# Optimization experiments

Measured on AMD Instinct MI355X. Metric: run time of the kernel, lower is better.

The kernel has to match this reference:

```python
import jax, jax.numpy as jnp
import numpy as np

B, NA, D, H = 64, 32, 128, 6  # scenes, agents/scene, out_dim, heads
N = B * NA
E = B * NA * NA


def layer_norm(x, g, b, eps=1e-5):
    m = jnp.mean(x, axis=-1, keepdims=True)
    v = jnp.var(x, axis=-1, keepdims=True)
    return (x - m) * jax.lax.rsqrt(v + eps) * g + b


def setup_inputs() -> dict:
    key = jax.random.key(0)
    ks = jax.random.split(key, 10)
    # fully-connected edges within each scene
    ids = jnp.arange(N, dtype=jnp.int32).reshape(B, NA)
    hi = jnp.broadcast_to(ids[:, :, None], (B, NA, NA)).reshape(-1)  # repeat 'd -> (d n)'
    wi = jnp.broadcast_to(ids[:, None, :], (B, NA, NA)).reshape(-1)  # repeat 'd -> (n d)'
    s_in = 1.0 / np.sqrt(D)
    s_hd = 1.0 / np.sqrt(H * D)
    return {
        'agents': jax.random.normal(ks[0], (N, D), jnp.float32),
        'hi': hi, 'wi': wi,
        'Wq': jax.random.normal(ks[1], (H * D, D), jnp.float32) * s_in,
        'gq': jnp.ones((H * D,), jnp.float32), 'bq': jnp.zeros((H * D,), jnp.float32),
        'Wk': jax.random.normal(ks[2], (H * D, D), jnp.float32) * s_in,
        'gk': jnp.ones((H * D,), jnp.float32), 'bk': jnp.zeros((H * D,), jnp.float32),
        'Wv': jax.random.normal(ks[3], (H * D, D), jnp.float32) * s_in,
        'gv': jnp.ones((H * D,), jnp.float32), 'bv': jnp.zeros((H * D,), jnp.float32),
        'Wo1': jax.random.normal(ks[4], (D, H * D), jnp.float32) * s_hd,
        'go': jnp.ones((D,), jnp.float32), 'bo': jnp.zeros((D,), jnp.float32),
        'Wo2': jax.random.normal(ks[5], (D, D), jnp.float32) * s_in,
        'W1': jax.random.normal(ks[6], (D, D), jnp.float32) * s_in,
        'gn': jnp.ones((D,), jnp.float32), 'bn': jnp.zeros((D,), jnp.float32),
        'W2': jax.random.normal(ks[7], (D, D), jnp.float32) * s_in,
    }


def reference(agents, hi, wi, Wq, gq, bq, Wk, gk, bk, Wv, gv, bv, Wo1, go, bo, Wo2, W1, gn, bn, W2):
    n, d = agents.shape
    scale = d ** -0.5
    xh = agents[hi]                                   # [E, D]
    xw = agents[wi]                                   # [E, D]
    q = layer_norm(xh @ Wq.T, gq, bq).reshape(-1, H, d)                 # [E, H, D]
    k = layer_norm(xw @ Wk.T, gk, bk).reshape(-1, H, d)
    v = jax.nn.relu(layer_norm(xw @ Wv.T, gv, bv)).reshape(-1, H, d)
    att = jnp.sum(q * k, axis=-1) * scale             # [E, H] per-edge score
    att = jnp.exp(att - jnp.max(att))                 # global max, as in original
    att_sum = jax.ops.segment_sum(att, hi, num_segments=n)   # [N, H]
    att = att / att_sum[hi]
    out = jax.ops.segment_sum(att[..., None] * v, hi, num_segments=n)   # [N, H, D]
    out = out.reshape(n, H * d)
    out = jax.nn.relu(layer_norm(out @ Wo1.T, go, bo)) @ Wo2.T          # to_out
    nodes = agents @ W1.T
    nodes = jax.nn.relu(layer_norm(nodes + out, gn, bn))
    nodes = nodes @ W2.T
    return jax.nn.relu(nodes + agents)
```

## Files before the change

kernel.cpp:

```cpp
#include <hip/hip_runtime.h>
#include <math.h>

#define NN 2048
#define HH 6
#define HD 768
#define NA 32
#define NB 64

typedef __bf16 bf16x8 __attribute__((ext_vector_type(8)));
typedef float  f32x4  __attribute__((ext_vector_type(4)));

__device__ __forceinline__ void split2(float f, ushort& h, ushort& l) {
    const uint u = __float_as_uint(f);
    h = (ushort)(u >> 16);
    const float hf = __uint_as_float((uint)h << 16);
    l = (ushort)(__float_as_uint(f - hf) >> 16);
}

__device__ __forceinline__ bf16x8 pack8(const ushort* s) {
    uint4 u;
    u.x = (uint)s[0] | ((uint)s[1] << 16);
    u.y = (uint)s[2] | ((uint)s[3] << 16);
    u.z = (uint)s[4] | ((uint)s[5] << 16);
    u.w = (uint)s[6] | ((uint)s[7] << 16);
    return *(bf16x8*)&u;
}

__device__ __forceinline__ void ln8_split(
    const float* __restrict__ x, float mu, float rs,
    const float* __restrict__ g, const float* __restrict__ b,
    bf16x8& hi, bf16x8& lo)
{
    const float4 x0 = *(const float4*)x;
    const float4 x1 = *(const float4*)(x + 4);
    const float4 g0 = *(const float4*)g;
    const float4 g1 = *(const float4*)(g + 4);
    const float4 b0 = *(const float4*)b;
    const float4 b1 = *(const float4*)(b + 4);
    ushort hh[8], ll[8];
    float v;
    v = (x0.x - mu) * rs * g0.x + b0.x; split2(v, hh[0], ll[0]);
    v = (x0.y - mu) * rs * g0.y + b0.y; split2(v, hh[1], ll[1]);
    v = (x0.z - mu) * rs * g0.z + b0.z; split2(v, hh[2], ll[2]);
    v = (x0.w - mu) * rs * g0.w + b0.w; split2(v, hh[3], ll[3]);
    v = (x1.x - mu) * rs * g1.x + b1.x; split2(v, hh[4], ll[4]);
    v = (x1.y - mu) * rs * g1.y + b1.y; split2(v, hh[5], ll[5]);
    v = (x1.z - mu) * rs * g1.z + b1.z; split2(v, hh[6], ll[6]);
    v = (x1.w - mu) * rs * g1.w + b1.w; split2(v, hh[7], ll[7]);
    hi = pack8(hh); lo = pack8(ll);
}

__global__ __launch_bounds__(256) void split_kernel(
    const float* __restrict__ agents, const float* __restrict__ Wq,
    const float* __restrict__ Wk, const float* __restrict__ Wv,
    const float* __restrict__ Wo1, const float* __restrict__ Wo2,
    const float* __restrict__ W1, const float* __restrict__ W2,
    ushort* __restrict__ Ahi, ushort* __restrict__ Alo,
    ushort* __restrict__ Whi, ushort* __restrict__ Wlo,
    ushort* __restrict__ Wo1hi, ushort* __restrict__ Wo1lo,
    ushort* __restrict__ Wo2hi, ushort* __restrict__ Wo2lo,
    ushort* __restrict__ W1hi, ushort* __restrict__ W1lo,
    ushort* __restrict__ W2hi, ushort* __restrict__ W2lo)
{
    const int y = blockIdx.y;
    const float* src;
    ushort *dh, *dl;
    int n4;
    switch (y) {
        case 0:  src = agents; dh = Ahi;   dl = Alo;   n4 = NN * 128 / 4;  break;
        case 1:  src = Wq;  dh = Whi;                dl = Wlo;                n4 = 768*128/4; break;
        case 2:  src = Wk;  dh = Whi + 768*128;      dl = Wlo + 768*128;      n4 = 768*128/4; break;
        case 3:  src = Wv;  dh = Whi + 2*768*128;    dl = Wlo + 2*768*128;    n4 = 768*128/4; break;
        case 4:  src = Wo1; dh = Wo1hi; dl = Wo1lo;  n4 = 128 * HD / 4;  break;
        case 5:  src = Wo2; dh = Wo2hi; dl = Wo2lo;  n4 = 128 * 128 / 4; break;
        case 6:  src = W1;  dh = W1hi;  dl = W1lo;   n4 = 128 * 128 / 4; break;
        default: src = W2;  dh = W2hi;  dl = W2lo;   n4 = 128 * 128 / 4; break;
    }
    const int i = blockIdx.x * 256 + threadIdx.x;
    if (i < n4) {
        const float4 v = ((const float4*)src)[i];
        ushort4 h, l;
        split2(v.x, h.x, l.x);
        split2(v.y, h.y, l.y);
        split2(v.z, h.z, l.z);
        split2(v.w, h.w, l.w);
        ((ushort4*)dh)[i] = h;
        ((ushort4*)dl)[i] = l;
    }
}

__global__ __launch_bounds__(256) void proj_mfma_kernel(
    const ushort* __restrict__ Ahi, const ushort* __restrict__ Alo,
    const ushort* __restrict__ Whi, const ushort* __restrict__ Wlo,
    float* __restrict__ R, float* __restrict__ ps)
{
    const int tid = threadIdx.x;
    const int wave = tid >> 6, lane = tid & 63;
    const int row0 = blockIdx.x * 64 + wave * 16;
    const int cb0  = blockIdx.y * 64;
    const int m0   = blockIdx.y / 12, pb = blockIdx.y % 12;
    const int lrow = lane & 15, kq = lane >> 4;
    const int koff = kq * 8;

    const ushort* ah = Ahi + (size_t)(row0 + lrow) * 128 + koff;
    const ushort* al = Alo + (size_t)(row0 + lrow) * 128 + koff;

    f32x4 acc[4];
    #pragma unroll
    for (int ct = 0; ct < 4; ++ct)
        #pragma unroll
        for (int j = 0; j < 4; ++j) acc[ct][j] = 0.f;

    #pragma unroll
    for (int kt = 0; kt < 4; ++kt) {
        const bf16x8 avh = *(const bf16x8*)(ah + kt * 32);
        const bf16x8 avl = *(const bf16x8*)(al + kt * 32);
        #pragma unroll
        for (int ct = 0; ct < 4; ++ct) {
            const size_t wof = (size_t)(cb0 + ct * 16 + lrow) * 128 + koff + kt * 32;
            const bf16x8 bvh = *(const bf16x8*)(Whi + wof);
            const bf16x8 bvl = *(const bf16x8*)(Wlo + wof);
            acc[ct] = __builtin_amdgcn_mfma_f32_16x16x32_bf16(avh, bvh, acc[ct], 0, 0, 0);
            acc[ct] = __builtin_amdgcn_mfma_f32_16x16x32_bf16(avh, bvl, acc[ct], 0, 0, 0);
            acc[ct] = __builtin_amdgcn_mfma_f32_16x16x32_bf16(avl, bvh, acc[ct], 0, 0, 0);
        }
    }

    const int cloc = cb0 - m0 * 768;
    #pragma unroll
    for (int ct = 0; ct < 4; ++ct) {
        const int c = cloc + ct * 16 + lrow;
        float* rp = R + ((size_t)m0 * NN + row0 + kq * 4) * HD + c;
        #pragma unroll
        for (int j = 0; j < 4; ++j)
            rp[(size_t)j * HD] = acc[ct][j];
    }

    #pragma unroll
    for (int j = 0; j < 4; ++j) {
        float sj = acc[0][j] + acc[1][j] + acc[2][j] + acc[3][j];
        float qj = acc[0][j] * acc[0][j] + acc[1][j] * acc[1][j]
                 + acc[2][j] * acc[2][j] + acc[3][j] * acc[3][j];
        #pragma unroll
        for (int msk = 1; msk <= 8; msk <<= 1) {
            sj += __shfl_xor(sj, msk);
            qj += __shfl_xor(qj, msk);
        }
        if (lrow == 0) {
            const size_t o = ((size_t)m0 * NN + row0 + kq * 4 + j) * 24 + pb * 2;
            ps[o]     = sj;
            ps[o + 1] = qj;
        }
    }
}

__global__ __launch_bounds__(64) void attn_mfma_kernel(
    const float* __restrict__ R, const float* __restrict__ ps,
    const float* __restrict__ gq, const float* __restrict__ bq,
    const float* __restrict__ gk, const float* __restrict__ bk,
    const float* __restrict__ gv, const float* __restrict__ bv,
    ushort* __restrict__ Ohi, ushort* __restrict__ Olo)
{
    __shared__ ushort phi[16][40];
    __shared__ ushort plo[16][40];
    __shared__ float stat_s[3][32][2];
    const int lane = threadIdx.x;
    const int lrow = lane & 15, kq = lane >> 4;
    const int scene = blockIdx.x, h = blockIdx.y, rt = blockIdx.z;
    const int brow = scene * 32;

    const float* Rq = R;
    const float* Rk = R + (size_t)NN * HD;
    const float* Rv = R + (size_t)2 * NN * HD;

    for (int i = lane; i < 96; i += 64) {
        const int m = i >> 5, row = i & 31;
        const float4* pv = (const float4*)(ps + ((size_t)m * NN + brow + row) * 24);
        float s = 0.f, q = 0.f;
        #pragma unroll
        for (int c = 0; c < 6; ++c) {
            const float4 v = pv[c];
            s += v.x + v.z;
            q += v.y + v.w;
        }
        const float mu  = s * (1.f / 768.f);
        const float var = q * (1.f / 768.f) - mu * mu;
        stat_s[m][row][0] = mu;
        stat_s[m][row][1] = rsqrtf(var + 1e-5f);
    }
    __syncthreads();

    const int qrow = brow + rt * 16 + lrow;
    const float muq = stat_s[0][rt * 16 + lrow][0];
    const float rsq = stat_s[0][rt * 16 + lrow][1];
    float muk[2], rsk[2];
    #pragma unroll
    for (int ct = 0; ct < 2; ++ct) {
        muk[ct] = stat_s[1][ct * 16 + lrow][0];
        rsk[ct] = stat_s[1][ct * 16 + lrow][1];
    }
    float muv[8], rsv[8];
    #pragma unroll
    for (int j = 0; j < 8; ++j) {
        muv[j] = stat_s[2][kq * 8 + j][0];
        rsv[j] = stat_s[2][kq * 8 + j][1];
    }

    f32x4 s[2];
    #pragma unroll
    for (int ct = 0; ct < 2; ++ct)
        #pragma unroll
        for (int j = 0; j < 4; ++j) s[ct][j] = 0.f;

    #pragma unroll
    for (int kt = 0; kt < 4; ++kt) {
        const int c0 = h * 128 + kt * 32 + kq * 8;
        bf16x8 qh, ql;
        ln8_split(Rq + (size_t)qrow * HD + c0, muq, rsq, gq + c0, bq + c0, qh, ql);
        #pragma unroll
        for (int ct = 0; ct < 2; ++ct) {
            bf16x8 kh, kl;
            ln8_split(Rk + (size_t)(brow + ct * 16 + lrow) * HD + c0, muk[ct], rsk[ct],
                      gk + c0, bk + c0, kh, kl);
            s[ct] = __builtin_amdgcn_mfma_f32_16x16x32_bf16(qh, kh, s[ct], 0, 0, 0);
            s[ct] = __builtin_amdgcn_mfma_f32_16x16x32_bf16(qh, kl, s[ct], 0, 0, 0);
            s[ct] = __builtin_amdgcn_mfma_f32_16x16x32_bf16(ql, kh, s[ct], 0, 0, 0);
        }
    }

    const float scl = 0.08838834764831845f;
    float p0[4], p1[4];
    #pragma unroll
    for (int j = 0; j < 4; ++j) {
        const float a = s[0][j] * scl, b = s[1][j] * scl;
        float m = fmaxf(a, b);
        #pragma unroll
        for (int msk = 1; msk <= 8; msk <<= 1) m = fmaxf(m, __shfl_xor(m, msk));
        const float ea = __expf(a - m), eb = __expf(b - m);
        float su = ea + eb;
        #pragma unroll
        for (int msk = 1; msk <= 8; msk <<= 1) su += __shfl_xor(su, msk);
        const float inv = 1.f / su;
        p0[j] = ea * inv;
        p1[j] = eb * inv;
    }

    #pragma unroll
    for (int j = 0; j < 4; ++j) {
        ushort hh, ll;
        split2(p0[j], hh, ll);
        phi[kq * 4 + j][lrow] = hh;
        plo[kq * 4 + j][lrow] = ll;
        split2(p1[j], hh, ll);
        phi[kq * 4 + j][16 + lrow] = hh;
        plo[kq * 4 + j][16 + lrow] = ll;
    }
    __syncthreads();
    const bf16x8 pah = *(const bf16x8*)&phi[lrow][kq * 8];
    const bf16x8 pal = *(const bf16x8*)&plo[lrow][kq * 8];

    #pragma unroll
    for (int dt = 0; dt < 8; ++dt) {
        const int d = h * 128 + dt * 16 + lrow;
        const float gvd = gv[d], bvd = bv[d];
        ushort vh[8], vl[8];
        #pragma unroll
        for (int j = 0; j < 8; ++j) {
            const float x = Rv[(size_t)(brow + kq * 8 + j) * HD + d];
            const float v = fmaxf((x - muv[j]) * rsv[j] * gvd + bvd, 0.f);
            split2(v, vh[j], vl[j]);
        }
        const bf16x8 bh = pack8(vh), bl = pack8(vl);
        f32x4 o;
        #pragma unroll
        for (int j = 0; j < 4; ++j) o[j] = 0.f;
        o = __builtin_amdgcn_mfma_f32_16x16x32_bf16(pah, bh, o, 0, 0, 0);
        o = __builtin_amdgcn_mfma_f32_16x16x32_bf16(pah, bl, o, 0, 0, 0);
        o = __builtin_amdgcn_mfma_f32_16x16x32_bf16(pal, bh, o, 0, 0, 0);
        #pragma unroll
        for (int j = 0; j < 4; ++j) {
            const size_t oo = (size_t)(brow + rt * 16 + kq * 4 + j) * HD + d;
            ushort hh, ll;
            split2(o[j], hh, ll);
            Ohi[oo] = hh;
            Olo[oo] = ll;
        }
    }
}

__global__ __launch_bounds__(256) void wo1_mfma_kernel(
    const ushort* __restrict__ Ohi, const ushort* __restrict__ Olo,
    const ushort* __restrict__ Wo1hi, const ushort* __restrict__ Wo1lo,
    float* __restrict__ P)
{
    const int tid = threadIdx.x;
    const int wave = tid >> 6, lane = tid & 63;
    const int row0 = blockIdx.x * 64 + wave * 16;
    const int col0 = blockIdx.y * 16;
    const int kb   = blockIdx.z * 256;
    const int lrow = lane & 15, kq = lane >> 4;
    const int koff = kq * 8;

    const ushort* ah = Ohi   + (size_t)(row0 + lrow) * HD + kb + koff;
    const ushort* al = Olo   + (size_t)(row0 + lrow) * HD + kb + koff;
    const ushort* bh = Wo1hi + (size_t)(col0 + lrow) * HD + kb + koff;
    const ushort* bl = Wo1lo + (size_t)(col0 + lrow) * HD + kb + koff;

    f32x4 acc;
    #pragma unroll
    for (int j = 0; j < 4; ++j) acc[j] = 0.f;

    #pragma unroll
    for (int kt = 0; kt < 8; ++kt) {
        const bf16x8 avh = *(const bf16x8*)(ah + kt * 32);
        const bf16x8 avl = *(const bf16x8*)(al + kt * 32);
        const bf16x8 bvh = *(const bf16x8*)(bh + kt * 32);
        const bf16x8 bvl = *(const bf16x8*)(bl + kt * 32);
        acc = __builtin_amdgcn_mfma_f32_16x16x32_bf16(avh, bvh, acc, 0, 0, 0);
        acc = __builtin_amdgcn_mfma_f32_16x16x32_bf16(avh, bvl, acc, 0, 0, 0);
        acc = __builtin_amdgcn_mfma_f32_16x16x32_bf16(avl, bvh, acc, 0, 0, 0);
    }

    float* pp = P + ((size_t)blockIdx.z * NN + row0 + kq * 4) * 128 + col0 + lrow;
    #pragma unroll
    for (int j = 0; j < 4; ++j)
        pp[(size_t)j * 128] = acc[j];
}

__global__ __launch_bounds__(256) void epilogue_mfma_kernel(
    const float* __restrict__ P,
    const ushort* __restrict__ Ahi, const ushort* __restrict__ Alo,
    const float* __restrict__ agents,
    const float* __restrict__ go, const float* __restrict__ bo,
    const ushort* __restrict__ Wo2hi, const ushort* __restrict__ Wo2lo,
    const ushort* __restrict__ W1hi, const ushort* __restrict__ W1lo,
    const float* __restrict__ gn, const float* __restrict__ bn,
    const ushort* __restrict__ W2hi, const ushort* __restrict__ W2lo,
    float* __restrict__ out)
{
    __shared__ float zb[16][132];
    __shared__ float red2[4][16][2];
    const int tid = threadIdx.x;
    const int wave = tid >> 6, lane = tid & 63;
    const int lrow = lane & 15, kq = lane >> 4;
    const int n0 = blockIdx.x * 16;
    const int nodeA = n0 + lrow;

    float tv[4][8];
    float s = 0.f, q = 0.f;
    #pragma unroll
    for (int kt = 0; kt < 4; ++kt) {
        const int c0 = kt * 32 + kq * 8;
        const float* pp0 = P + (size_t)nodeA * 128 + c0;
        const float* pp1 = pp0 + (size_t)NN * 128;
        const float* pp2 = pp1 + (size_t)NN * 128;
        #pragma unroll
        for (int hf = 0; hf < 2; ++hf) {
            const float4 a = *(const float4*)(pp0 + hf * 4);
            const float4 b = *(const float4*)(pp1 + hf * 4);
            const float4 c = *(const float4*)(pp2 + hf * 4);
            tv[kt][hf * 4 + 0] = a.x + b.x + c.x;
            tv[kt][hf * 4 + 1] = a.y + b.y + c.y;
            tv[kt][hf * 4 + 2] = a.z + b.z + c.z;
            tv[kt][hf * 4 + 3] = a.w + b.w + c.w;
        }
        #pragma unroll
        for (int j = 0; j < 8; ++j) { s += tv[kt][j]; q += tv[kt][j] * tv[kt][j]; }
    }
    s += __shfl_xor(s, 16); s += __shfl_xor(s, 32);
    q += __shfl_xor(q, 16); q += __shfl_xor(q, 32);
    const float mu = s * (1.f / 128.f);
    const float rs = rsqrtf(q * (1.f / 128.f) - mu * mu + 1e-5f);

    bf16x8 th[4], tl[4], ah[4], al[4];
    #pragma unroll
    for (int kt = 0; kt < 4; ++kt) {
        const int c0 = kt * 32 + kq * 8;
        const float4 g0 = *(const float4*)(go + c0);
        const float4 g1 = *(const float4*)(go + c0 + 4);
        const float4 b0 = *(const float4*)(bo + c0);
        const float4 b1 = *(const float4*)(bo + c0 + 4);
        const float gg[8] = {g0.x, g0.y, g0.z, g0.w, g1.x, g1.y, g1.z, g1.w};
        const float bb[8] = {b0.x, b0.y, b0.z, b0.w, b1.x, b1.y, b1.z, b1.w};
        ushort hh[8], ll[8];
        #pragma unroll
        for (int j = 0; j < 8; ++j) {
            const float v = fmaxf((tv[kt][j] - mu) * rs * gg[j] + bb[j], 0.f);
            split2(v, hh[j], ll[j]);
        }
        th[kt] = pack8(hh); tl[kt] = pack8(ll);
        ah[kt] = *(const bf16x8*)(Ahi + (size_t)nodeA * 128 + c0);
        al[kt] = *(const bf16x8*)(Alo + (size_t)nodeA * 128 + c0);
    }

    f32x4 u[2];
    #pragma unroll
    for (int ct2 = 0; ct2 < 2; ++ct2)
        #pragma unroll
        for (int j = 0; j < 4; ++j) u[ct2][j] = 0.f;

    #pragma unroll
    for (int ct2 = 0; ct2 < 2; ++ct2) {
        const int ct = wave * 2 + ct2;
        const size_t wb = (size_t)(ct * 16 + lrow) * 128;
        #pragma unroll
        for (int kt = 0; kt < 4; ++kt) {
            const int c0 = kt * 32 + kq * 8;
            const bf16x8 wh = *(const bf16x8*)(Wo2hi + wb + c0);
            const bf16x8 wl = *(const bf16x8*)(Wo2lo + wb + c0);
            const bf16x8 vh = *(const bf16x8*)(W1hi + wb + c0);
            const bf16x8 vl = *(const bf16x8*)(W1lo + wb + c0);
            u[ct2] = __builtin_amdgcn_mfma_f32_16x16x32_bf16(th[kt], wh, u[ct2], 0, 0, 0);
            u[ct2] = __builtin_amdgcn_mfma_f32_16x16x32_bf16(th[kt], wl, u[ct2], 0, 0, 0);
            u[ct2] = __builtin_amdgcn_mfma_f32_16x16x32_bf16(tl[kt], wh, u[ct2], 0, 0, 0);
            u[ct2] = __builtin_amdgcn_mfma_f32_16x16x32_bf16(ah[kt], vh, u[ct2], 0, 0, 0);
            u[ct2] = __builtin_amdgcn_mfma_f32_16x16x32_bf16(ah[kt], vl, u[ct2], 0, 0, 0);
            u[ct2] = __builtin_amdgcn_mfma_f32_16x16x32_bf16(al[kt], vh, u[ct2], 0, 0, 0);
        }
    }

    #pragma unroll
    for (int j = 0; j < 4; ++j) {
        float s2 = u[0][j] + u[1][j];
        float q2 = u[0][j] * u[0][j] + u[1][j] * u[1][j];
        #pragma unroll
        for (int msk = 1; msk <= 8; msk <<= 1) {
            s2 += __shfl_xor(s2, msk);
            q2 += __shfl_xor(q2, msk);
        }
        if (lrow == 0) {
            red2[wave][kq * 4 + j][0] = s2;
            red2[wave][kq * 4 + j][1] = q2;
        }
    }
    __syncthreads();
    #pragma unroll
    for (int j = 0; j < 4; ++j) {
        const int row = kq * 4 + j;
        const float s2t = red2[0][row][0] + red2[1][row][0] + red2[2][row][0] + red2[3][row][0];
        const float q2t = red2[0][row][1] + red2[1][row][1] + red2[2][row][1] + red2[3][row][1];
        const float mu2 = s2t * (1.f / 128.f);
        const float rs2 = rsqrtf(q2t * (1.f / 128.f) - mu2 * mu2 + 1e-5f);
        #pragma unroll
        for (int ct2 = 0; ct2 < 2; ++ct2) {
            const int c = (wave * 2 + ct2) * 16 + lrow;
            zb[row][c] = fmaxf((u[ct2][j] - mu2) * rs2 * gn[c] + bn[c], 0.f);
        }
    }
    __syncthreads();

    bf16x8 zh[4], zl[4];
    #pragma unroll
    for (int kt = 0; kt < 4; ++kt) {
        const int c0 = kt * 32 + kq * 8;
        const float4 z0 = *(const float4*)&zb[lrow][c0];
        const float4 z1 = *(const float4*)&zb[lrow][c0 + 4];
        const float zz[8] = {z0.x, z0.y, z0.z, z0.w, z1.x, z1.y, z1.z, z1.w};
        ushort hh[8], ll[8];
        #pragma unroll
        for (int j = 0; j < 8; ++j) split2(zz[j], hh[j], ll[j]);
        zh[kt] = pack8(hh); zl[kt] = pack8(ll);
    }
    #pragma unroll
    for (int ct2 = 0; ct2 < 2; ++ct2) {
        const int ct = wave * 2 + ct2;
        f32x4 o;
        #pragma unroll
        for (int j = 0; j < 4; ++j) o[j] = 0.f;
        const size_t wb = (size_t)(ct * 16 + lrow) * 128;
        #pragma unroll
        for (int kt = 0; kt < 4; ++kt) {
            const int c0 = kt * 32 + kq * 8;
            const bf16x8 wh = *(const bf16x8*)(W2hi + wb + c0);
            const bf16x8 wl = *(const bf16x8*)(W2lo + wb + c0);
            o = __builtin_amdgcn_mfma_f32_16x16x32_bf16(zh[kt], wh, o, 0, 0, 0);
            o = __builtin_amdgcn_mfma_f32_16x16x32_bf16(zh[kt], wl, o, 0, 0, 0);
            o = __builtin_amdgcn_mfma_f32_16x16x32_bf16(zl[kt], wh, o, 0, 0, 0);
        }
        #pragma unroll
        for (int j = 0; j < 4; ++j) {
            const size_t oo = (size_t)(n0 + kq * 4 + j) * 128 + ct * 16 + lrow;
            out[oo] = fmaxf(o[j] + agents[oo], 0.f);
        }
    }
}

extern "C" void kernel_launch(void* const* d_in, const int* in_sizes, int n_in,
                              void* d_out, int out_size, void* d_ws, size_t ws_size,
                              hipStream_t stream) {
    (void)in_sizes; (void)n_in; (void)out_size; (void)ws_size;
    const float* agents = (const float*)d_in[0];
    const float* Wq  = (const float*)d_in[3];
    const float* gq  = (const float*)d_in[4];
    const float* bq  = (const float*)d_in[5];
    const float* Wk  = (const float*)d_in[6];
    const float* gk  = (const float*)d_in[7];
    const float* bk  = (const float*)d_in[8];
    const float* Wv  = (const float*)d_in[9];
    const float* gv  = (const float*)d_in[10];
    const float* bv  = (const float*)d_in[11];
    const float* Wo1 = (const float*)d_in[12];
    const float* go  = (const float*)d_in[13];
    const float* bo  = (const float*)d_in[14];
    const float* Wo2 = (const float*)d_in[15];
    const float* W1  = (const float*)d_in[16];
    const float* gn  = (const float*)d_in[17];
    const float* bn  = (const float*)d_in[18];
    const float* W2  = (const float*)d_in[19];
    float* out = (float*)d_out;

    float* ws = (float*)d_ws;
    float* R  = ws;
    float* Pp = R;
    float* ps = R + (size_t)3 * NN * HD;
    ushort* u = (ushort*)(ps + (size_t)3 * NN * 24);
    ushort* Ohi   = u;  u += (size_t)NN * HD;
    ushort* Olo   = u;  u += (size_t)NN * HD;
    ushort* Ahi   = u;  u += (size_t)NN * 128;
    ushort* Alo   = u;  u += (size_t)NN * 128;
    ushort* Whi   = u;  u += (size_t)3 * 768 * 128;
    ushort* Wlo   = u;  u += (size_t)3 * 768 * 128;
    ushort* Wo1hi = u;  u += (size_t)128 * HD;
    ushort* Wo1lo = u;  u += (size_t)128 * HD;
    ushort* Wo2hi = u;  u += (size_t)128 * 128;
    ushort* Wo2lo = u;  u += (size_t)128 * 128;
    ushort* W1hi  = u;  u += (size_t)128 * 128;
    ushort* W1lo  = u;  u += (size_t)128 * 128;
    ushort* W2hi  = u;  u += (size_t)128 * 128;
    ushort* W2lo  = u;  u += (size_t)128 * 128;

    split_kernel<<<dim3(256, 8), 256, 0, stream>>>(
        agents, Wq, Wk, Wv, Wo1, Wo2, W1, W2,
        Ahi, Alo, Whi, Wlo, Wo1hi, Wo1lo, Wo2hi, Wo2lo, W1hi, W1lo, W2hi, W2lo);
    proj_mfma_kernel<<<dim3(32, 36), 256, 0, stream>>>(Ahi, Alo, Whi, Wlo, R, ps);
    attn_mfma_kernel<<<dim3(64, 6, 2), 64, 0, stream>>>(R, ps, gq, bq, gk, bk, gv, bv, Ohi, Olo);
    wo1_mfma_kernel<<<dim3(32, 8, 3), 256, 0, stream>>>(Ohi, Olo, Wo1hi, Wo1lo, Pp);
    epilogue_mfma_kernel<<<128, 256, 0, stream>>>(Pp, Ahi, Alo, agents, go, bo,
                                                  Wo2hi, Wo2lo, W1hi, W1lo, gn, bn,
                                                  W2hi, W2lo, out);
}
```

Measured before the change: 160.4 us.

## Fuse attention output with per-head Wo1 projection, emitting per-head partials

Merges the attention kernel and the Wo1 GEMM into one kernel. Each block, one scene and one head with two waves of 16 query rows, keeps the attention output in shared memory, splits it to hi/lo bf16 and multiplies by that head's 128-column slice of Wo1. The Ohi/Olo round trip through global memory and a kernel launch are removed. In exchange the epilogue now sums six per-head partial buffers instead of three, and Wo1 is reread by every scene block.

```diff
diff --git a/kernel.cpp b/kernel.cpp
--- a/kernel.cpp
+++ b/kernel.cpp
@@ -154,27 +154,30 @@
     }
 }
 
-__global__ __launch_bounds__(64) void attn_mfma_kernel(
+__global__ __launch_bounds__(128) void attn_wo1_kernel(
     const float* __restrict__ R, const float* __restrict__ ps,
     const float* __restrict__ gq, const float* __restrict__ bq,
     const float* __restrict__ gk, const float* __restrict__ bk,
     const float* __restrict__ gv, const float* __restrict__ bv,
-    ushort* __restrict__ Ohi, ushort* __restrict__ Olo)
+    const ushort* __restrict__ Wo1hi, const ushort* __restrict__ Wo1lo,
+    float* __restrict__ P)
 {
-    __shared__ ushort phi[16][40];
-    __shared__ ushort plo[16][40];
     __shared__ float stat_s[3][32][2];
-    const int lane = threadIdx.x;
+    __shared__ ushort phi[2][16][40];
+    __shared__ ushort plo[2][16][40];
+    __shared__ float ob[2][16][140];
+    const int tid = threadIdx.x;
+    const int rt = tid >> 6, lane = tid & 63;
     const int lrow = lane & 15, kq = lane >> 4;
-    const int scene = blockIdx.x, h = blockIdx.y, rt = blockIdx.z;
+    const int scene = blockIdx.x, h = blockIdx.y;
     const int brow = scene * 32;
 
     const float* Rq = R;
     const float* Rk = R + (size_t)NN * HD;
     const float* Rv = R + (size_t)2 * NN * HD;
 
-    for (int i = lane; i < 96; i += 64) {
-        const int m = i >> 5, row = i & 31;
+    if (tid < 96) {
+        const int m = tid >> 5, row = tid & 31;
         const float4* pv = (const float4*)(ps + ((size_t)m * NN + brow + row) * 24);
         float s = 0.f, q = 0.f;
         #pragma unroll
@@ -249,16 +252,17 @@
     for (int j = 0; j < 4; ++j) {
         ushort hh, ll;
         split2(p0[j], hh, ll);
-        phi[kq * 4 + j][lrow] = hh;
-        plo[kq * 4 + j][lrow] = ll;
+        phi[rt][kq * 4 + j][lrow] = hh;
+        plo[rt][kq * 4 + j][lrow] = ll;
         split2(p1[j], hh, ll);
-        phi[kq * 4 + j][16 + lrow] = hh;
-        plo[kq * 4 + j][16 + lrow] = ll;
+        phi[rt][kq * 4 + j][16 + lrow] = hh;
+        plo[rt][kq * 4 + j][16 + lrow] = ll;
     }
     __syncthreads();
-    const bf16x8 pah = *(const bf16x8*)&phi[lrow][kq * 8];
-    const bf16x8 pal = *(const bf16x8*)&plo[lrow][kq * 8];
-
+    const bf16x8 pah = *(const bf16x8*)&phi[rt][lrow][kq * 8];
+    const bf16x8 pal = *(const bf16x8*)&plo[rt][lrow][kq * 8];
+
+    f32x4 o[8];
     #pragma unroll
     for (int dt = 0; dt < 8; ++dt) {
         const int d = h * 128 + dt * 16 + lrow;
@@ -271,60 +275,52 @@
             split2(v, vh[j], vl[j]);
         }
         const bf16x8 bh = pack8(vh), bl = pack8(vl);
-        f32x4 o;
-        #pragma unroll
-        for (int j = 0; j < 4; ++j) o[j] = 0.f;
-        o = __builtin_amdgcn_mfma_f32_16x16x32_bf16(pah, bh, o, 0, 0, 0);
-        o = __builtin_amdgcn_mfma_f32_16x16x32_bf16(pah, bl, o, 0, 0, 0);
-        o = __builtin_amdgcn_mfma_f32_16x16x32_bf16(pal, bh, o, 0, 0, 0);
-        #pragma unroll
-        for (int j = 0; j < 4; ++j) {
-            const size_t oo = (size_t)(brow + rt * 16 + kq * 4 + j) * HD + d;
-            ushort hh, ll;
-            split2(o[j], hh, ll);
-            Ohi[oo] = hh;
-            Olo[oo] = ll;
-        }
-    }
-}
-
-__global__ __launch_bounds__(256) void wo1_mfma_kernel(
-    const ushort* __restrict__ Ohi, const ushort* __restrict__ Olo,
-    const ushort* __restrict__ Wo1hi, const ushort* __restrict__ Wo1lo,
-    float* __restrict__ P)
-{
-    const int tid = threadIdx.x;
-    const int wave = tid >> 6, lane = tid & 63;
-    const int row0 = blockIdx.x * 64 + wave * 16;
-    const int col0 = blockIdx.y * 16;
-    const int kb   = blockIdx.z * 256;
-    const int lrow = lane & 15, kq = lane >> 4;
-    const int koff = kq * 8;
-
-    const ushort* ah = Ohi   + (size_t)(row0 + lrow) * HD + kb + koff;
-    const ushort* al = Olo   + (size_t)(row0 + lrow) * HD + kb + koff;
-    const ushort* bh = Wo1hi + (size_t)(col0 + lrow) * HD + kb + koff;
-    const ushort* bl = Wo1lo + (size_t)(col0 + lrow) * HD + kb + koff;
-
-    f32x4 acc;
-    #pragma unroll
-    for (int j = 0; j < 4; ++j) acc[j] = 0.f;
-
-    #pragma unroll
-    for (int kt = 0; kt < 8; ++kt) {
-        const bf16x8 avh = *(const bf16x8*)(ah + kt * 32);
-        const bf16x8 avl = *(const bf16x8*)(al + kt * 32);
-        const bf16x8 bvh = *(const bf16x8*)(bh + kt * 32);
-        const bf16x8 bvl = *(const bf16x8*)(bl + kt * 32);
-        acc = __builtin_amdgcn_mfma_f32_16x16x32_bf16(avh, bvh, acc, 0, 0, 0);
-        acc = __builtin_amdgcn_mfma_f32_16x16x32_bf16(avh, bvl, acc, 0, 0, 0);
-        acc = __builtin_amdgcn_mfma_f32_16x16x32_bf16(avl, bvh, acc, 0, 0, 0);
-    }
-
-    float* pp = P + ((size_t)blockIdx.z * NN + row0 + kq * 4) * 128 + col0 + lrow;
-    #pragma unroll
-    for (int j = 0; j < 4; ++j)
-        pp[(size_t)j * 128] = acc[j];
+        #pragma unroll
+        for (int j = 0; j < 4; ++j) o[dt][j] = 0.f;
+        o[dt] = __builtin_amdgcn_mfma_f32_16x16x32_bf16(pah, bh, o[dt], 0, 0, 0);
+        o[dt] = __builtin_amdgcn_mfma_f32_16x16x32_bf16(pah, bl, o[dt], 0, 0, 0);
+        o[dt] = __builtin_amdgcn_mfma_f32_16x16x32_bf16(pal, bh, o[dt], 0, 0, 0);
+    }
+
+    #pragma unroll
+    for (int dt = 0; dt < 8; ++dt)
+        #pragma unroll
+        for (int j = 0; j < 4; ++j)
+            ob[rt][kq * 4 + j][dt * 16 + lrow] = o[dt][j];
+    __syncthreads();
+
+    bf16x8 oh[4], ol[4];
+    #pragma unroll
+    for (int kt = 0; kt < 4; ++kt) {
+        const float4 z0 = *(const float4*)&ob[rt][lrow][kt * 32 + kq * 8];
+        const float4 z1 = *(const float4*)&ob[rt][lrow][kt * 32 + kq * 8 + 4];
+        const float zz[8] = {z0.x, z0.y, z0.z, z0.w, z1.x, z1.y, z1.z, z1.w};
+        ushort hh[8], ll[8];
+        #pragma unroll
+        for (int j = 0; j < 8; ++j) split2(zz[j], hh[j], ll[j]);
+        oh[kt] = pack8(hh); ol[kt] = pack8(ll);
+    }
+
+    #pragma unroll
+    for (int ct = 0; ct < 8; ++ct) {
+        f32x4 p2;
+        #pragma unroll
+        for (int j = 0; j < 4; ++j) p2[j] = 0.f;
+        const size_t wb = (size_t)(ct * 16 + lrow) * HD + h * 128;
+        #pragma unroll
+        for (int kt = 0; kt < 4; ++kt) {
+            const int c0 = kt * 32 + kq * 8;
+            const bf16x8 wh = *(const bf16x8*)(Wo1hi + wb + c0);
+            const bf16x8 wl = *(const bf16x8*)(Wo1lo + wb + c0);
+            p2 = __builtin_amdgcn_mfma_f32_16x16x32_bf16(oh[kt], wh, p2, 0, 0, 0);
+            p2 = __builtin_amdgcn_mfma_f32_16x16x32_bf16(oh[kt], wl, p2, 0, 0, 0);
+            p2 = __builtin_amdgcn_mfma_f32_16x16x32_bf16(ol[kt], wh, p2, 0, 0, 0);
+        }
+        float* pp = P + ((size_t)h * NN + brow + rt * 16 + kq * 4) * 128 + ct * 16 + lrow;
+        #pragma unroll
+        for (int j = 0; j < 4; ++j)
+            pp[(size_t)j * 128] = p2[j];
+    }
 }
 
 __global__ __launch_bounds__(256) void epilogue_mfma_kernel(
@@ -351,18 +347,19 @@
     #pragma unroll
     for (int kt = 0; kt < 4; ++kt) {
         const int c0 = kt * 32 + kq * 8;
-        const float* pp0 = P + (size_t)nodeA * 128 + c0;
-        const float* pp1 = pp0 + (size_t)NN * 128;
-        const float* pp2 = pp1 + (size_t)NN * 128;
+        const size_t base = (size_t)nodeA * 128 + c0;
         #pragma unroll
         for (int hf = 0; hf < 2; ++hf) {
-            const float4 a = *(const float4*)(pp0 + hf * 4);
-            const float4 b = *(const float4*)(pp1 + hf * 4);
-            const float4 c = *(const float4*)(pp2 + hf * 4);
-            tv[kt][hf * 4 + 0] = a.x + b.x + c.x;
-            tv[kt][hf * 4 + 1] = a.y + b.y + c.y;
-            tv[kt][hf * 4 + 2] = a.z + b.z + c.z;
-            tv[kt][hf * 4 + 3] = a.w + b.w + c.w;
+            float ax = 0.f, ay = 0.f, az = 0.f, aw = 0.f;
+            #pragma unroll
+            for (int head = 0; head < 6; ++head) {
+                const float4 v = *(const float4*)(P + (size_t)head * NN * 128 + base + hf * 4);
+                ax += v.x; ay += v.y; az += v.z; aw += v.w;
+            }
+            tv[kt][hf * 4 + 0] = ax;
+            tv[kt][hf * 4 + 1] = ay;
+            tv[kt][hf * 4 + 2] = az;
+            tv[kt][hf * 4 + 3] = aw;
         }
         #pragma unroll
         for (int j = 0; j < 8; ++j) { s += tv[kt][j]; q += tv[kt][j] * tv[kt][j]; }
@@ -511,11 +508,9 @@
 
     float* ws = (float*)d_ws;
     float* R  = ws;
-    float* Pp = R;
-    float* ps = R + (size_t)3 * NN * HD;
+    float* Pp = R + (size_t)3 * NN * HD;
+    float* ps = Pp + (size_t)6 * NN * 128;
     ushort* u = (ushort*)(ps + (size_t)3 * NN * 24);
-    ushort* Ohi   = u;  u += (size_t)NN * HD;
-    ushort* Olo   = u;  u += (size_t)NN * HD;
     ushort* Ahi   = u;  u += (size_t)NN * 128;
     ushort* Alo   = u;  u += (size_t)NN * 128;
     ushort* Whi   = u;  u += (size_t)3 * 768 * 128;
@@ -533,8 +528,8 @@
         agents, Wq, Wk, Wv, Wo1, Wo2, W1, W2,
         Ahi, Alo, Whi, Wlo, Wo1hi, Wo1lo, Wo2hi, Wo2lo, W1hi, W1lo, W2hi, W2lo);
     proj_mfma_kernel<<<dim3(32, 36), 256, 0, stream>>>(Ahi, Alo, Whi, Wlo, R, ps);
-    attn_mfma_kernel<<<dim3(64, 6, 2), 64, 0, stream>>>(R, ps, gq, bq, gk, bk, gv, bv, Ohi, Olo);
-    wo1_mfma_kernel<<<dim3(32, 8, 3), 256, 0, stream>>>(Ohi, Olo, Wo1hi, Wo1lo, Pp);
+    attn_wo1_kernel<<<dim3(NB, HH), 128, 0, stream>>>(R, ps, gq, bq, gk, bk, gv, bv,
+                                                      Wo1hi, Wo1lo, Pp);
     epilogue_mfma_kernel<<<128, 256, 0, stream>>>(Pp, Ahi, Alo, agents, go, bo,
                                                   Wo2hi, Wo2lo, W1hi, W1lo, gn, bn,
                                                   W2hi, W2lo, out);
```

Measured after the change: 159.8 us. Within noise of the previous version (-0.4%).
